# Kernel optimization log

Hardware: AMD Instinct MI355X
Metric: run time of the kernel (lower is better)

Reference implementation:

```python
import jax, jax.numpy as jnp
import numpy as np

D_MODEL = 1024
NUM_HEADS = 16
HEAD_DIM = D_MODEL // NUM_HEADS  # 64
# NOTE: the torch module passes scale=attention_head_size (NOT 1/sqrt(dh));
# we reproduce that exact math: scores are MULTIPLIED by head_dim.
SCALE = float(HEAD_DIM)

B, S = 2, 2048


def setup_inputs() -> dict:
    key = jax.random.key(0)
    ks = jax.random.split(key, 6)
    q = jax.random.normal(ks[0], (B, S, D_MODEL), dtype=jnp.float32)
    k = jax.random.normal(ks[1], (B, S, D_MODEL), dtype=jnp.float32)
    v = jax.random.normal(ks[2], (B, S, D_MODEL), dtype=jnp.float32)
    # Linear weights stored as [in, out]; scaled like typical init so the
    # (head_dim-scaled) logits stay numerically sane.
    w_std = 0.02
    Wq = jax.random.normal(ks[3], (D_MODEL, D_MODEL), dtype=jnp.float32) * w_std
    Wk = jax.random.normal(ks[4], (D_MODEL, D_MODEL), dtype=jnp.float32) * w_std
    Wv = jax.random.normal(ks[5], (D_MODEL, D_MODEL), dtype=jnp.float32) * w_std
    return {"q": q, "k": k, "v": v, "Wq": Wq, "Wk": Wk, "Wv": Wv}


def reference(q, k, v, Wq, Wk, Wv):
    Bq, Sq, _ = q.shape
    # QKV projections (qkv_bias=False), split into heads: [B, S, H, dh]
    qh = (q @ Wq).reshape(Bq, Sq, NUM_HEADS, HEAD_DIM)
    kh = (k @ Wk).reshape(Bq, Sq, NUM_HEADS, HEAD_DIM)
    vh = (v @ Wv).reshape(Bq, Sq, NUM_HEADS, HEAD_DIM)
    # Full materialized scores [B, H, Sq, Sk] -- the naive MHA pattern.
    sims = jnp.einsum("bqhd,bkhd->bhqk", qh, kh) * SCALE
    attn = jax.nn.softmax(sims, axis=-1)
    # Second matmul, then merge heads back: [B, S, D]
    out = jnp.einsum("bhqk,bkhd->bqhd", attn, vh).reshape(Bq, Sq, D_MODEL)
    return out
```

## Files before the change

### kernel.cpp

```cpp
#include <hip/hip_runtime.h>
#include <cstdint>
#include <cstddef>

typedef unsigned short u16;
typedef __bf16 bf16x8 __attribute__((ext_vector_type(8)));
typedef float f32x4 __attribute__((ext_vector_type(4)));
typedef unsigned int u32x4 __attribute__((ext_vector_type(4)));
typedef unsigned int u32x2 __attribute__((ext_vector_type(2)));
typedef u16 u16x4 __attribute__((ext_vector_type(4)));

typedef __attribute__((address_space(3))) void lds_void;
typedef __attribute__((address_space(1))) void glb_void;

constexpr float CEXP = 92.33248261689366f;

constexpr size_t XSZ = 4096ull * 1024ull;
constexpr size_t WSZ = 1024ull * 1024ull;
constexpr size_t OFF_WQH = 0;
constexpr size_t OFF_WQL = OFF_WQH + WSZ;
constexpr size_t OFF_WKH = OFF_WQL + WSZ;
constexpr size_t OFF_WKL = OFF_WKH + WSZ;
constexpr size_t OFF_WVH = OFF_WKL + WSZ;
constexpr size_t OFF_WVL = OFF_WVH + WSZ;
constexpr size_t OFF_QH  = OFF_WVL + WSZ;
constexpr size_t OFF_QL  = OFF_QH + XSZ;
constexpr size_t OFF_KH  = OFF_QL + XSZ;
constexpr size_t OFF_KL  = OFF_KH + XSZ;
constexpr size_t OFF_VT  = OFF_KL + XSZ;

__device__ __forceinline__ u16 f2b(float f) {
  unsigned u = __builtin_bit_cast(unsigned, f);
  return (u16)((u + 0x7FFFu + ((u >> 16) & 1u)) >> 16);
}
__device__ __forceinline__ float b2f(u16 h) {
  return __builtin_bit_cast(float, ((unsigned)h) << 16);
}
__device__ __forceinline__ float bitf(unsigned u) {
  return __builtin_bit_cast(float, u);
}
__device__ __forceinline__ bf16x8 ld8(const u16* p) {
  return __builtin_bit_cast(bf16x8, *(const u32x4*)p);
}
__device__ __forceinline__ unsigned pk2(float a, float b) {
#if __has_builtin(__builtin_amdgcn_cvt_pk_bf16_f32)
  auto v = __builtin_amdgcn_cvt_pk_bf16_f32(a, b);
  return __builtin_bit_cast(unsigned, v);
#else
  return (unsigned)f2b(a) | ((unsigned)f2b(b) << 16);
#endif
}
__device__ __forceinline__ float ex2(float x) {
#if __has_builtin(__builtin_amdgcn_exp2f)
  return __builtin_amdgcn_exp2f(x);
#else
  return exp2f(x);
#endif
}
__device__ __forceinline__ void glds16(const void* g, void* l) {
  __builtin_amdgcn_global_load_lds((const glb_void*)g, (lds_void*)l, 16, 0, 0);
}
__device__ __forceinline__ int swz32(int row, int cg) {
  return row * 32 + ((cg ^ ((row >> 1) & 3)) * 8);
}
__device__ __forceinline__ int swz64(int row, int cg) {
  return row * 64 + ((cg ^ (row & 7)) * 8);
}

__global__ __launch_bounds__(256) void convert_w(const float* __restrict__ Wq,
                                                 const float* __restrict__ Wk,
                                                 const float* __restrict__ Wv,
                                                 u16* __restrict__ ws) {
  __shared__ float tile[32][33];
  int id = blockIdx.x;
  int t = threadIdx.x;
  int z = id >> 10, rem = id & 1023;
  const float* W = (z == 0) ? Wq : (z == 1) ? Wk : Wv;
  u16* hiT = ws + ((z == 0) ? OFF_WQH : (z == 1) ? OFF_WKH : OFF_WVH);
  u16* loT = ws + ((z == 0) ? OFF_WQL : (z == 1) ? OFF_WKL : OFF_WVL);
  int n0 = (rem & 31) * 32, k0 = (rem >> 5) * 32;
  int r = t >> 3, c0 = (t & 7) * 4;
  float4 vv = *(const float4*)(W + (size_t)(k0 + r) * 1024 + n0 + c0);
  tile[r][c0] = vv.x; tile[r][c0 + 1] = vv.y; tile[r][c0 + 2] = vv.z; tile[r][c0 + 3] = vv.w;
  __syncthreads();
  u16x4 hv, lv;
#pragma unroll
  for (int j = 0; j < 4; ++j) {
    float x = tile[c0 + j][r];
    u16 hb = f2b(x);
    hv[j] = hb;
    lv[j] = f2b(x - b2f(hb));
  }
  size_t o = (size_t)(n0 + r) * 1024 + k0 + c0;
  *(u16x4*)(hiT + o) = hv;
  if (z != 2) *(u16x4*)(loT + o) = lv;
}

__global__ __launch_bounds__(256, 3) void gemm_qkv(u16* __restrict__ ws,
                                                   const float* __restrict__ xq,
                                                   const float* __restrict__ xk,
                                                   const float* __restrict__ xv) {
  __shared__ u16 smem[16384];
  float* sAf = (float*)smem;
  u16* sBh = smem + 8192;
  u16* sBl = smem + 12288;
  u16* cbuf = smem;

  int id = blockIdx.x;
  int xcd = id & 7, seq = id >> 3;
  int pair = (seq >> 3) * 8 + xcd;
  int tile_n = seq & 7;
  int z = pair >> 5;
  int tile_m = pair & 31;

  const float* X = (z == 0) ? xq : (z == 1) ? xk : xv;
  const u16 *Bh, *Bl; u16 *Oh, *Ol; bool split;
  if (z == 0)      { Bh = ws + OFF_WQH; Bl = ws + OFF_WQL; Oh = ws + OFF_QH; Ol = ws + OFF_QL; split = true; }
  else if (z == 1) { Bh = ws + OFF_WKH; Bl = ws + OFF_WKL; Oh = ws + OFF_KH; Ol = ws + OFF_KL; split = true; }
  else             { Bh = ws + OFF_WVH; Bl = nullptr;      Oh = ws + OFF_VT; Ol = nullptr;    split = false; }
  float oscale = (z == 0) ? CEXP : 1.0f;
  int m0 = tile_m * 128, n0 = tile_n * 128;
  int t = threadIdx.x, lane = t & 63, wave = t >> 6;
  int quad = lane >> 4, l15 = lane & 15;
  int wm = (wave >> 1) * 64, wn = (wave & 1) * 64;
  int rl = lane >> 2, cgl = lane & 3;
  int rt = t >> 3, ct = t & 7;
  f32x4 acc[4][4] = {};

  size_t gAf[4]; int lbAf[4];
#pragma unroll
  for (int i = 0; i < 4; ++i) {
    int row = i * 32 + rt;
    gAf[i] = (size_t)(m0 + row) * 1024 + ((ct ^ (row & 7)) * 4);
    lbAf[i] = (i * 256 + t) * 4;
  }
  size_t gB[2]; int lbB[2];
#pragma unroll
  for (int i = 0; i < 2; ++i) {
    int rowB = wave * 32 + i * 16 + rl;
    gB[i] = (size_t)(n0 + rowB) * 1024 + (cgl ^ ((rowB >> 1) & 3)) * 8;
    lbB[i] = wave * 1024 + i * 512;
  }
  int soAf[4][2];
#pragma unroll
  for (int mt = 0; mt < 4; ++mt) {
    int ra = wm + mt * 16 + l15;
    soAf[mt][0] = ra * 32 + (((2 * quad) ^ (ra & 7)) * 4);
    soAf[mt][1] = ra * 32 + (((2 * quad + 1) ^ (ra & 7)) * 4);
  }

  for (int kb = 0; kb < 32; ++kb) {
    int k0 = kb * 32;
    __syncthreads();
#pragma unroll
    for (int i = 0; i < 4; ++i)
      glds16(X + gAf[i] + k0, sAf + lbAf[i]);
#pragma unroll
    for (int i = 0; i < 2; ++i) {
      glds16(Bh + gB[i] + k0, &sBh[lbB[i]]);
      if (split) glds16(Bl + gB[i] + k0, &sBl[lbB[i]]);
    }
    __syncthreads();
    bf16x8 afh[4], afl[4];
#pragma unroll
    for (int mt = 0; mt < 4; ++mt) {
      f32x4 a0 = *(const f32x4*)(sAf + soAf[mt][0]);
      f32x4 a1 = *(const f32x4*)(sAf + soAf[mt][1]);
      u32x4 hw;
      hw[0] = pk2(a0[0], a0[1]); hw[1] = pk2(a0[2], a0[3]);
      hw[2] = pk2(a1[0], a1[1]); hw[3] = pk2(a1[2], a1[3]);
      afh[mt] = __builtin_bit_cast(bf16x8, hw);
      if (split) {
        u32x4 lw;
        lw[0] = pk2(a0[0] - bitf(hw[0] << 16), a0[1] - bitf(hw[0] & 0xFFFF0000u));
        lw[1] = pk2(a0[2] - bitf(hw[1] << 16), a0[3] - bitf(hw[1] & 0xFFFF0000u));
        lw[2] = pk2(a1[0] - bitf(hw[2] << 16), a1[1] - bitf(hw[2] & 0xFFFF0000u));
        lw[3] = pk2(a1[2] - bitf(hw[3] << 16), a1[3] - bitf(hw[3] & 0xFFFF0000u));
        afl[mt] = __builtin_bit_cast(bf16x8, lw);
      }
    }
#pragma unroll
    for (int nt = 0; nt < 4; ++nt) {
      int rb = wn + nt * 16 + l15;
      bf16x8 bfh = ld8(&sBh[swz32(rb, quad)]);
      bf16x8 bfl;
      if (split) bfl = ld8(&sBl[swz32(rb, quad)]);
#pragma unroll
      for (int mt = 0; mt < 4; ++mt) {
        acc[mt][nt] = __builtin_amdgcn_mfma_f32_16x16x32_bf16(afh[mt], bfh, acc[mt][nt], 0, 0, 0);
        if (split) {
          acc[mt][nt] = __builtin_amdgcn_mfma_f32_16x16x32_bf16(afl[mt], bfh, acc[mt][nt], 0, 0, 0);
          acc[mt][nt] = __builtin_amdgcn_mfma_f32_16x16x32_bf16(afh[mt], bfl, acc[mt][nt], 0, 0, 0);
        }
      }
    }
  }
  auto epi_round = [&](u16* dst, bool lo_round) {
#pragma unroll
    for (int mt = 0; mt < 4; ++mt)
#pragma unroll
      for (int nt = 0; nt < 4; ++nt)
#pragma unroll
        for (int r = 0; r < 4; ++r) {
          int row = wm + mt * 16 + quad * 4 + r;
          int col = wn + nt * 16 + l15;
          float v = acc[mt][nt][r] * oscale;
          u16 hb = f2b(v);
          u16 val = lo_round ? f2b(v - b2f(hb)) : hb;
          cbuf[row * 128 + (((col >> 3) ^ (row & 15)) * 8) + (col & 7)] = val;
        }
    __syncthreads();
#pragma unroll
    for (int rr = 0; rr < 2; ++rr) {
      int row = rr * 64 + (t >> 2), seg = t & 3;
      int gm = m0 + row, bb = gm >> 11, s = gm & 2047;
      int hh = (n0 >> 6) + (seg >> 1), d0 = (seg & 1) * 32;
      u16* gp = dst + ((size_t)(bb * 16 + hh) * 2048 + s) * 64 + d0;
#pragma unroll
      for (int i = 0; i < 4; ++i) {
        int phys = (seg * 4 + i) ^ (row & 15);
        *(u32x4*)(gp + i * 8) = *(const u32x4*)(&cbuf[row * 128 + phys * 8]);
      }
    }
  };
  __syncthreads();
  if (split) {
    epi_round(Oh, false);
    __syncthreads();
    epi_round(Ol, true);
  } else {
#pragma unroll
    for (int mt = 0; mt < 4; ++mt)
#pragma unroll
      for (int nt = 0; nt < 4; ++nt)
#pragma unroll
        for (int r = 0; r < 4; ++r) {
          int row = wm + mt * 16 + quad * 4 + r;
          int col = wn + nt * 16 + l15;
          cbuf[row * 128 + (((col >> 3) ^ (row & 15)) * 8) + (col & 7)] =
              f2b(acc[mt][nt][r]);
        }
    __syncthreads();
    int col = t >> 1, sh = t & 1;
    int hg = (n0 + col) >> 6, d = (n0 + col) & 63;
    int bb = m0 >> 11, s0 = m0 & 2047;
#pragma unroll
    for (int part = 0; part < 2; ++part) {
      u16 vals[32];
#pragma unroll
      for (int i = 0; i < 32; ++i) {
        int row = part * 64 + sh * 32 + i;
        vals[i] = cbuf[row * 128 + (((col >> 3) ^ (row & 15)) * 8) + (col & 7)];
      }
      u16* gp = Oh + ((size_t)((bb * 16 + hg) * 64 + d)) * 2048 + s0 + part * 64 + sh * 32;
#pragma unroll
      for (int i = 0; i < 4; ++i)
        *(u32x4*)(gp + i * 8) = *(const u32x4*)(&vals[i * 8]);
    }
  }
}

__global__ __launch_bounds__(256, 4) void attn(const u16* __restrict__ ws,
                                               float* __restrict__ out) {
  __shared__ u16 lkh[64 * 64];
  __shared__ u16 lkl[64 * 64];
  __shared__ u16 lvt[2][64 * 64];
  __shared__ u16 lp[4][16 * 64];
  const u16* Qh = ws + OFF_QH; const u16* Ql = ws + OFF_QL;
  const u16* Kh = ws + OFF_KH; const u16* Kl = ws + OFF_KL;
  const u16* Vt = ws + OFF_VT;
  int id = blockIdx.x;
  int xcd = id & 7, slot = id >> 3;
  int hh = xcd * 4 + (slot >> 5);
  int q0 = (slot & 31) * 64;
  int b = hh >> 4, h = hh & 15;
  int t = threadIdx.x, lane = t & 63, wave = t >> 6;
  int quad = lane >> 4, l15 = lane & 15;
  size_t hb = (size_t)hh * (2048 * 64);
  bf16x8 onesf;
#pragma unroll
  for (int j = 0; j < 8; ++j) onesf[j] = __builtin_bit_cast(__bf16, (u16)0x3F80);
  int qrow = q0 + wave * 16 + l15;
  bf16x8 qfh[2], qfl[2];
#pragma unroll
  for (int ks = 0; ks < 2; ++ks) {
    size_t qo = hb + (size_t)qrow * 64 + ks * 32 + quad * 8;
    qfh[ks] = ld8(Qh + qo);
    qfl[ks] = ld8(Ql + qo);
  }
  float mi = -1e30f;
  f32x4 lsum = {};
  f32x4 o[4] = {};
  int rl = lane >> 3, cgl = lane & 7;

  size_t aK[2], aV[2]; int lb[2];
#pragma unroll
  for (int i = 0; i < 2; ++i) {
    int row = wave * 16 + i * 8 + rl;
    int cgg = cgl ^ (row & 7);
    aK[i] = hb + (size_t)row * 64 + cgg * 8;
    aV[i] = hb + (size_t)row * 2048 + cgg * 8;
    lb[i] = (wave * 16 + i * 8) * 64;
  }
  int soF[2][4];
#pragma unroll
  for (int ks = 0; ks < 2; ++ks)
#pragma unroll
    for (int nt = 0; nt < 4; ++nt)
      soF[ks][nt] = swz64(nt * 16 + l15, ks * 4 + quad);
  int soP[4];
  {
    int r7 = l15 & 7;
#pragma unroll
    for (int nt = 0; nt < 4; ++nt) {
      int c = nt * 2 + (quad >> 1);
      soP[nt] = l15 * 64 + ((c ^ r7) * 8) + (quad & 1) * 4;
    }
  }
  int soPa[2];
#pragma unroll
  for (int ks = 0; ks < 2; ++ks) soPa[ks] = swz64(l15, ks * 4 + quad);
  u16* lpw = &lp[wave][0];

#pragma unroll
  for (int i = 0; i < 2; ++i) {
    glds16(Kh + aK[i], &lkh[lb[i]]);
    glds16(Kl + aK[i], &lkl[lb[i]]);
    glds16(Vt + aV[i], &lvt[0][lb[i]]);
  }
  u32x4 pk_[2], pl_[2], pv_[2];
#pragma unroll
  for (int i = 0; i < 2; ++i) {
    pk_[i] = *(const u32x4*)(Kh + aK[i] + 4096);
    pl_[i] = *(const u32x4*)(Kl + aK[i] + 4096);
    pv_[i] = *(const u32x4*)(Vt + aV[i] + 64);
  }
  __syncthreads();

  for (int kt = 0; kt < 32; ++kt) {
    f32x4 sc[4] = {};
    __builtin_amdgcn_s_setprio(1);
#pragma unroll
    for (int nt = 0; nt < 4; ++nt) {
#pragma unroll
      for (int ks = 0; ks < 2; ++ks) {
        bf16x8 kh_ = ld8(&lkh[soF[ks][nt]]);
        bf16x8 kl_ = ld8(&lkl[soF[ks][nt]]);
        sc[nt] = __builtin_amdgcn_mfma_f32_16x16x32_bf16(kh_, qfh[ks], sc[nt], 0, 0, 0);
        sc[nt] = __builtin_amdgcn_mfma_f32_16x16x32_bf16(kl_, qfh[ks], sc[nt], 0, 0, 0);
        sc[nt] = __builtin_amdgcn_mfma_f32_16x16x32_bf16(kh_, qfl[ks], sc[nt], 0, 0, 0);
      }
    }
    __builtin_amdgcn_s_setprio(0);
    __syncthreads();
    if (kt < 31) {
#pragma unroll
      for (int i = 0; i < 2; ++i) {
        *(u32x4*)(&lkh[lb[i] + lane * 8]) = pk_[i];
        *(u32x4*)(&lkl[lb[i] + lane * 8]) = pl_[i];
        *(u32x4*)(&lvt[(kt + 1) & 1][lb[i] + lane * 8]) = pv_[i];
      }
    }
    __syncthreads();
    if (kt < 30) {
#pragma unroll
      for (int i = 0; i < 2; ++i) {
        pk_[i] = *(const u32x4*)(Kh + aK[i] + (kt + 2) * 4096);
        pl_[i] = *(const u32x4*)(Kl + aK[i] + (kt + 2) * 4096);
        pv_[i] = *(const u32x4*)(Vt + aV[i] + (kt + 2) * 64);
      }
    }
    float t0 = fmaxf(fmaxf(sc[0][0], sc[0][1]), sc[0][2]);
    float t1 = fmaxf(fmaxf(sc[0][3], sc[1][0]), sc[1][1]);
    float t2 = fmaxf(fmaxf(sc[1][2], sc[1][3]), sc[2][0]);
    float t3 = fmaxf(fmaxf(sc[2][1], sc[2][2]), sc[2][3]);
    float t4 = fmaxf(fmaxf(sc[3][0], sc[3][1]), sc[3][2]);
    float mx = fmaxf(fmaxf(fmaxf(t0, t1), fmaxf(t2, t3)), fmaxf(t4, sc[3][3]));
    mx = fmaxf(mx, __shfl_xor(mx, 16));
    mx = fmaxf(mx, __shfl_xor(mx, 32));
    float mi_old = mi;
    unsigned long long live = __ballot(mx > mi_old - 28.0f);
    float mn = fmaxf(mi_old, mx);
    mi = mn;
    if (live) {
      unsigned long long grew = __ballot(mx > mi_old);
#pragma unroll
      for (int nt = 0; nt < 4; ++nt) {
        unsigned u01 = pk2(ex2(sc[nt][0] - mn), ex2(sc[nt][1] - mn));
        unsigned u23 = pk2(ex2(sc[nt][2] - mn), ex2(sc[nt][3] - mn));
        *(u32x2*)(&lpw[soP[nt]]) = u32x2{u01, u23};
      }
      if (grew) {
        float a = ex2(mi_old - mn);
#pragma unroll
        for (int r = 0; r < 4; ++r) {
          lsum[r] *= a;
          o[0][r] *= a; o[1][r] *= a; o[2][r] *= a; o[3][r] *= a;
        }
      }
      asm volatile("s_waitcnt lgkmcnt(0)" ::: "memory");
      bf16x8 pa[2];
#pragma unroll
      for (int ks = 0; ks < 2; ++ks) pa[ks] = ld8(&lpw[soPa[ks]]);
      __builtin_amdgcn_s_setprio(1);
      lsum = __builtin_amdgcn_mfma_f32_16x16x32_bf16(onesf, pa[0], lsum, 0, 0, 0);
      lsum = __builtin_amdgcn_mfma_f32_16x16x32_bf16(onesf, pa[1], lsum, 0, 0, 0);
      const u16* lv = &lvt[kt & 1][0];
#pragma unroll
      for (int nt = 0; nt < 4; ++nt)
#pragma unroll
        for (int ks = 0; ks < 2; ++ks) {
          bf16x8 bv = ld8(&lv[soF[ks][nt]]);
          o[nt] = __builtin_amdgcn_mfma_f32_16x16x32_bf16(bv, pa[ks], o[nt], 0, 0, 0);
        }
      __builtin_amdgcn_s_setprio(0);
    }
  }
  float inv = 1.0f / lsum[0];
  float* op = out + (size_t)(b * 2048 + q0 + wave * 16 + l15) * 1024 + h * 64;
#pragma unroll
  for (int nt = 0; nt < 4; ++nt) {
    f32x4 w;
#pragma unroll
    for (int r = 0; r < 4; ++r) w[r] = o[nt][r] * inv;
    *(f32x4*)(op + nt * 16 + quad * 4) = w;
  }
}

extern "C" void kernel_launch(void* const* d_in, const int* in_sizes, int n_in,
                              void* d_out, int out_size, void* d_ws, size_t ws_size,
                              hipStream_t stream) {
  const float* q  = (const float*)d_in[0];
  const float* k  = (const float*)d_in[1];
  const float* v  = (const float*)d_in[2];
  const float* Wq = (const float*)d_in[3];
  const float* Wk = (const float*)d_in[4];
  const float* Wv = (const float*)d_in[5];
  u16* ws = (u16*)d_ws;
  float* out = (float*)d_out;

  convert_w<<<3072, 256, 0, stream>>>(Wq, Wk, Wv, ws);
  gemm_qkv<<<768, 256, 0, stream>>>(ws, q, k, v);
  attn<<<1024, 256, 0, stream>>>(ws, out);
}
```

Baseline: 272.7 us.

## Register-prefetch QKV GEMM tiles and convert A to bf16 hi/lo once at LDS store

Replaces the direct global-to-LDS loads in the QKV projection GEMM with register-staged prefetch: the tiles for step kb+2 are loaded into registers while step kb computes, then committed to LDS. The fp32 A tile is split into bf16 hi/lo once per element when written to LDS, instead of every wave redoing the conversion after its LDS read. The goal is to hide global load latency and cut repeated conversion ALU work. In exchange it uses more VGPRs for the staging buffers, which could lower occupancy under launch_bounds(256,3), and it adds a commit phase between two barriers.

```diff
diff --git a/kernel.cpp b/kernel.cpp
--- a/kernel.cpp
+++ b/kernel.cpp
@@ -100,7 +100,8 @@
                                                    const float* __restrict__ xk,
                                                    const float* __restrict__ xv) {
   __shared__ u16 smem[16384];
-  float* sAf = (float*)smem;
+  u16* sAh = smem;
+  u16* sAl = smem + 4096;
   u16* sBh = smem + 8192;
   u16* sBl = smem + 12288;
   u16* cbuf = smem;
@@ -122,61 +123,61 @@
   int t = threadIdx.x, lane = t & 63, wave = t >> 6;
   int quad = lane >> 4, l15 = lane & 15;
   int wm = (wave >> 1) * 64, wn = (wave & 1) * 64;
-  int rl = lane >> 2, cgl = lane & 3;
-  int rt = t >> 3, ct = t & 7;
   f32x4 acc[4][4] = {};
 
-  size_t gAf[4]; int lbAf[4];
-#pragma unroll
-  for (int i = 0; i < 4; ++i) {
-    int row = i * 32 + rt;
-    gAf[i] = (size_t)(m0 + row) * 1024 + ((ct ^ (row & 7)) * 4);
-    lbAf[i] = (i * 256 + t) * 4;
-  }
-  size_t gB[2]; int lbB[2];
-#pragma unroll
-  for (int i = 0; i < 2; ++i) {
-    int rowB = wave * 32 + i * 16 + rl;
-    gB[i] = (size_t)(n0 + rowB) * 1024 + (cgl ^ ((rowB >> 1) & 3)) * 8;
-    lbB[i] = wave * 1024 + i * 512;
-  }
-  int soAf[4][2];
-#pragma unroll
-  for (int mt = 0; mt < 4; ++mt) {
-    int ra = wm + mt * 16 + l15;
-    soAf[mt][0] = ra * 32 + (((2 * quad) ^ (ra & 7)) * 4);
-    soAf[mt][1] = ra * 32 + (((2 * quad + 1) ^ (ra & 7)) * 4);
-  }
+  int sr = t & 127, skh = t >> 7;
+  const float* aSrc = X + (size_t)(m0 + sr) * 1024 + skh * 16;
+  const u16* bhSrc = Bh + (size_t)(n0 + sr) * 1024 + skh * 16;
+  const u16* blSrc = split ? (Bl + (size_t)(n0 + sr) * 1024 + skh * 16) : nullptr;
+  int so0 = swz32(sr, skh * 2), so1 = swz32(sr, skh * 2 + 1);
+
+  float4 xa[4]; u32x4 xbh[2], xbl[2];
+  auto issue = [&](int kb) {
+    const float* ap = aSrc + kb * 32;
+#pragma unroll
+    for (int i = 0; i < 4; ++i) xa[i] = *(const float4*)(ap + i * 4);
+    const u16* bp = bhSrc + kb * 32;
+    xbh[0] = *(const u32x4*)(bp);
+    xbh[1] = *(const u32x4*)(bp + 8);
+    if (split) {
+      const u16* lp = blSrc + kb * 32;
+      xbl[0] = *(const u32x4*)(lp);
+      xbl[1] = *(const u32x4*)(lp + 8);
+    }
+  };
+  auto commit = [&]() {
+    unsigned hw[8], lw[8];
+#pragma unroll
+    for (int p = 0; p < 8; ++p) {
+      float a0 = xa[p >> 1][(p & 1) * 2];
+      float a1 = xa[p >> 1][(p & 1) * 2 + 1];
+      hw[p] = pk2(a0, a1);
+      lw[p] = pk2(a0 - bitf(hw[p] << 16), a1 - bitf(hw[p] & 0xFFFF0000u));
+    }
+    *(u32x4*)(&sAh[so0]) = u32x4{hw[0], hw[1], hw[2], hw[3]};
+    *(u32x4*)(&sAh[so1]) = u32x4{hw[4], hw[5], hw[6], hw[7]};
+    *(u32x4*)(&sBh[so0]) = xbh[0];
+    *(u32x4*)(&sBh[so1]) = xbh[1];
+    if (split) {
+      *(u32x4*)(&sAl[so0]) = u32x4{lw[0], lw[1], lw[2], lw[3]};
+      *(u32x4*)(&sAl[so1]) = u32x4{lw[4], lw[5], lw[6], lw[7]};
+      *(u32x4*)(&sBl[so0]) = xbl[0];
+      *(u32x4*)(&sBl[so1]) = xbl[1];
+    }
+  };
+
+  issue(0);
+  commit();
+  issue(1);
+  __syncthreads();
 
   for (int kb = 0; kb < 32; ++kb) {
-    int k0 = kb * 32;
-    __syncthreads();
-#pragma unroll
-    for (int i = 0; i < 4; ++i)
-      glds16(X + gAf[i] + k0, sAf + lbAf[i]);
-#pragma unroll
-    for (int i = 0; i < 2; ++i) {
-      glds16(Bh + gB[i] + k0, &sBh[lbB[i]]);
-      if (split) glds16(Bl + gB[i] + k0, &sBl[lbB[i]]);
-    }
-    __syncthreads();
     bf16x8 afh[4], afl[4];
 #pragma unroll
     for (int mt = 0; mt < 4; ++mt) {
-      f32x4 a0 = *(const f32x4*)(sAf + soAf[mt][0]);
-      f32x4 a1 = *(const f32x4*)(sAf + soAf[mt][1]);
-      u32x4 hw;
-      hw[0] = pk2(a0[0], a0[1]); hw[1] = pk2(a0[2], a0[3]);
-      hw[2] = pk2(a1[0], a1[1]); hw[3] = pk2(a1[2], a1[3]);
-      afh[mt] = __builtin_bit_cast(bf16x8, hw);
-      if (split) {
-        u32x4 lw;
-        lw[0] = pk2(a0[0] - bitf(hw[0] << 16), a0[1] - bitf(hw[0] & 0xFFFF0000u));
-        lw[1] = pk2(a0[2] - bitf(hw[1] << 16), a0[3] - bitf(hw[1] & 0xFFFF0000u));
-        lw[2] = pk2(a1[0] - bitf(hw[2] << 16), a1[1] - bitf(hw[2] & 0xFFFF0000u));
-        lw[3] = pk2(a1[2] - bitf(hw[3] << 16), a1[3] - bitf(hw[3] & 0xFFFF0000u));
-        afl[mt] = __builtin_bit_cast(bf16x8, lw);
-      }
+      int ra = wm + mt * 16 + l15;
+      afh[mt] = ld8(&sAh[swz32(ra, quad)]);
+      if (split) afl[mt] = ld8(&sAl[swz32(ra, quad)]);
     }
 #pragma unroll
     for (int nt = 0; nt < 4; ++nt) {
@@ -193,7 +194,12 @@
         }
       }
     }
-  }
+    __syncthreads();
+    if (kb < 31) commit();
+    __syncthreads();
+    if (kb < 30) issue(kb + 2);
+  }
+
   auto epi_round = [&](u16* dst, bool lo_round) {
 #pragma unroll
     for (int mt = 0; mt < 4; ++mt)
```

After: 315.3 us. +15.6%, slower.
